# Kernel tuning notes

Measured on AMD Instinct MI355X. Metric: run time of the kernel, lower is better.

Reference implementation:

```python
import jax, jax.numpy as jnp
import numpy as np

N_HEADS = 4
IN_FEATURES = 1024


def setup_inputs() -> dict:
    key = jax.random.key(0)
    ks = jax.random.split(key, 20)
    B, HW, C = 2, 16384, 1024
    inp = {
        "q": jax.random.normal(ks[0], (B, HW, C), dtype=jnp.float32),
        "k": jax.random.normal(ks[1], (B, HW, C), dtype=jnp.float32),
        "v": jax.random.normal(ks[2], (B, HW, C), dtype=jnp.float32),
    }
    names = ["wqg", "bqg", "wkg", "bkg", "wvg", "bvg",
             "wql", "bql", "wkl", "bkl", "wvl", "bvl", "wp", "bp"]
    for i, n in enumerate(names):
        inp[n] = jax.random.normal(ks[3 + i], (C,), dtype=jnp.float32)
    return inp


def _channel_attention(qm, km, vm, scale):
    # qm/km/vm: (b, hw, c). Attention over the CHANNEL dim per head.
    b, n, c = qm.shape
    d = c // N_HEADS
    qh = qm.reshape(b, n, N_HEADS, d).transpose(0, 2, 3, 1)  # (b, H, d, hw)
    kh = km.reshape(b, n, N_HEADS, d).transpose(0, 2, 3, 1)
    vh = vm.reshape(b, n, N_HEADS, d).transpose(0, 2, 3, 1)
    scores = jnp.einsum("bhdn,bhen->bhde", qh, kh) * scale  # (b, H, d, d)
    attn = jax.nn.softmax(scores, axis=-1)
    out = jnp.einsum("bhde,bhen->bhdn", attn, vh)            # (b, H, d, hw)
    return out.transpose(0, 3, 1, 2).reshape(b, n, c)        # (b, hw, c)


def reference(q, k, v, wqg, bqg, wkg, bkg, wvg, bvg,
              wql, bql, wkl, bkl, wvl, bvl, wp, bp):
    scale = IN_FEATURES ** (-0.5)
    # Depthwise (groups==channels, kernel=1) projections: per-channel affine.
    att_global = _channel_attention(q * wqg + bqg, k * wkg + bkg, v * wvg + bvg, scale)
    # window_size=1 -> local patch extraction is identity; local branch uses its own maps.
    att_local = _channel_attention(q * wql + bql, k * wkl + bkl, v * wvl + bvl, scale)
    att = att_global + att_local
    # Both accumulators hold the same att, so projection input is 2*att.
    return (2.0 * att) * wp + bp
```

## Files before the change

kernel.cpp:

```cpp
#include <hip/hip_runtime.h>
#include <stdint.h>

#define NTOK 16384
#define CDIM 1024
#define DHEAD 256

typedef short s16x8 __attribute__((ext_vector_type(8)));
typedef unsigned short u16x8 __attribute__((ext_vector_type(8)));
typedef _Float16 h16x8 __attribute__((ext_vector_type(8)));
typedef float f32x4 __attribute__((ext_vector_type(4)));
typedef float f32x16 __attribute__((ext_vector_type(16)));

static __device__ __forceinline__ unsigned short f2bf(float f) {
    union { float f; unsigned u; } x; x.f = f;
    unsigned r = (x.u + 0x7fffu + ((x.u >> 16) & 1u)) >> 16;
    return (unsigned short)r;
}
static __device__ __forceinline__ unsigned short f2h(float f) {
    _Float16 h = (_Float16)f;
    return __builtin_bit_cast(unsigned short, h);
}
static __device__ __forceinline__ void lgkm_barrier() {
    asm volatile("s_waitcnt lgkmcnt(0)" ::: "memory");
    __builtin_amdgcn_s_barrier();
}

__global__ __launch_bounds__(512, 4)
void k_gram(const float* __restrict__ q, const float* __restrict__ k,
            unsigned short* __restrict__ Gpart, float* __restrict__ Spart, int nchunk)
{
    __shared__ __align__(16) unsigned short ls[(256 + 128) * 32];
    unsigned short* lq = ls;
    unsigned short* lk = ls + 256 * 32;

    const int t      = threadIdx.x;
    const int eh     = blockIdx.x & 1;
    const int pairid = blockIdx.x >> 1;
    const int bh     = pairid / nchunk;
    const int chunk  = pairid - bh * nchunk;
    const int b      = bh >> 2, h = bh & 3;
    const int rows   = NTOK / nchunk;
    const int S      = rows >> 5;
    const int n0c    = chunk * rows;

    const int lane = t & 63, w = t >> 6;
    const int wr = w >> 1;
    const int wc = w & 1;
    const int l31 = lane & 31, g2 = lane >> 5;

    const int qcq = t >> 3, qrg = t & 7;
    const int kcq = t >> 4, krs = t & 15;

    const float* qp = q + ((size_t)b * NTOK + n0c + qrg * 4) * CDIM + h * DHEAD + qcq * 4;
    const float* kp = k + ((size_t)b * NTOK + n0c + krs * 2) * CDIM + h * DHEAD + eh * 128 + kcq * 4;

    f32x4 qv[4], kv[2];
#define QLOAD(sidx) do { const size_t o_ = (size_t)(sidx) * 32 * CDIM;            \
        qv[0] = *reinterpret_cast<const f32x4*>(qp + o_);                          \
        qv[1] = *reinterpret_cast<const f32x4*>(qp + o_ + CDIM);                   \
        qv[2] = *reinterpret_cast<const f32x4*>(qp + o_ + 2 * CDIM);               \
        qv[3] = *reinterpret_cast<const f32x4*>(qp + o_ + 3 * CDIM); } while (0)
#define KLOAD(sidx) do { const size_t o_ = (size_t)(sidx) * 32 * CDIM;            \
        kv[0] = *reinterpret_cast<const f32x4*>(kp + o_);                          \
        kv[1] = *reinterpret_cast<const f32x4*>(kp + o_ + CDIM); } while (0)

    QLOAD(0);
    KLOAD(0);

    float sq[4] = {0.f, 0.f, 0.f, 0.f}, sk[4] = {0.f, 0.f, 0.f, 0.f};
    f32x16 acc[2][2];
#pragma unroll
    for (int r = 0; r < 2; ++r)
#pragma unroll
        for (int c = 0; c < 2; ++c)
#pragma unroll
            for (int j = 0; j < 16; ++j) acc[r][c][j] = 0.f;

    for (int s = 0; s < S; ++s) {
#pragma unroll
        for (int j = 0; j < 4; ++j) {
            const int ch = qcq * 4 + j;
            ushort4 p;
            p.x = f2bf(qv[0][j]); p.y = f2bf(qv[1][j]);
            p.z = f2bf(qv[2][j]); p.w = f2bf(qv[3][j]);
            sq[j] += (qv[0][j] + qv[1][j]) + (qv[2][j] + qv[3][j]);
            *reinterpret_cast<ushort4*>(
                &lq[ch * 32 + (((qrg >> 1) ^ (qcq & 3)) * 8) + (qrg & 1) * 4]) = p;
        }
        if (s + 1 < S) QLOAD(s + 1);

#pragma unroll
        for (int j = 0; j < 4; ++j) {
            const int ch = kcq * 4 + j;
            const unsigned pk = (unsigned)f2bf(kv[0][j]) | ((unsigned)f2bf(kv[1][j]) << 16);
            sk[j] += kv[0][j] + kv[1][j];
            *reinterpret_cast<unsigned*>(
                &lk[ch * 32 + (((krs >> 2) ^ (kcq & 3)) * 8) + (krs & 3) * 2]) = pk;
        }
        if (s + 1 < S) KLOAD(s + 1);

        lgkm_barrier();

#pragma unroll
        for (int kk = 0; kk < 2; ++kk) {
            s16x8 af[2];
#pragma unroll
            for (int r = 0; r < 2; ++r) {
                const int ch   = wr * 64 + r * 32 + l31;
                const int slot = (kk * 2 + g2) ^ ((ch >> 2) & 3);
                af[r] = *reinterpret_cast<const s16x8*>(&lq[ch * 32 + slot * 8]);
            }
#pragma unroll
            for (int c = 0; c < 2; ++c) {
                const int ch   = wc * 64 + c * 32 + l31;
                const int slot = (kk * 2 + g2) ^ ((ch >> 2) & 3);
                const s16x8 bf = *reinterpret_cast<const s16x8*>(&lk[ch * 32 + slot * 8]);
#pragma unroll
                for (int r = 0; r < 2; ++r)
                    acc[r][c] = __builtin_amdgcn_mfma_f32_32x32x16_bf16(af[r], bf, acc[r][c], 0, 0, 0);
            }
        }
        lgkm_barrier();
    }
#undef QLOAD
#undef KLOAD

#pragma unroll
    for (int off = 1; off < 8; off <<= 1)
#pragma unroll
        for (int j = 0; j < 4; ++j) sq[j] += __shfl_xor(sq[j], off);
#pragma unroll
    for (int off = 1; off < 16; off <<= 1)
#pragma unroll
        for (int j = 0; j < 4; ++j) sk[j] += __shfl_xor(sk[j], off);
    float* sp = Spart + (size_t)(bh * nchunk + chunk) * 512;
    if ((t & 7) == 0)
        *reinterpret_cast<float4*>(&sp[qcq * 4]) = make_float4(sq[0], sq[1], sq[2], sq[3]);
    if ((t & 15) == 0)
        *reinterpret_cast<float4*>(&sp[256 + eh * 128 + kcq * 4]) = make_float4(sk[0], sk[1], sk[2], sk[3]);

    unsigned short* gp = Gpart + (size_t)(bh * nchunk + chunk) * 65536;
#pragma unroll
    for (int qtr = 0; qtr < 4; ++qtr) {
        if (wr == qtr) {
#pragma unroll
            for (int r = 0; r < 2; ++r)
#pragma unroll
                for (int c = 0; c < 2; ++c)
#pragma unroll
                    for (int reg = 0; reg < 16; ++reg) {
                        const int de_l = r * 32 + (reg & 3) + 8 * (reg >> 2) + 4 * g2;
                        const int e_l  = wc * 64 + c * 32 + l31;
                        ls[de_l * 128 + e_l] = f2h(acc[r][c][reg]);
                    }
        }
        lgkm_barrier();
        {
            const int de_r = t >> 3, col = (t & 7) * 16;
            unsigned short* dst = gp + (qtr * 64 + de_r) * 256 + eh * 128 + col;
            *reinterpret_cast<u16x8*>(dst)     = *reinterpret_cast<const u16x8*>(&ls[de_r * 128 + col]);
            *reinterpret_cast<u16x8*>(dst + 8) = *reinterpret_cast<const u16x8*>(&ls[de_r * 128 + col + 8]);
        }
        lgkm_barrier();
    }
}

__global__ __launch_bounds__(256)
void k_scores(const unsigned short* __restrict__ Gpart, const float* __restrict__ Spart,
              const float* __restrict__ wqg, const float* __restrict__ bqg,
              const float* __restrict__ wkg, const float* __restrict__ bkg,
              const float* __restrict__ wvg, const float* __restrict__ bvg,
              const float* __restrict__ wql, const float* __restrict__ bql,
              const float* __restrict__ wkl, const float* __restrict__ bkl,
              const float* __restrict__ wvl, const float* __restrict__ bvl,
              const float* __restrict__ wp,  const float* __restrict__ bp,
              unsigned short* __restrict__ Wf, float* __restrict__ beta, int nchunk)
{
    __shared__ float sSq[256], sSk[256];
    const int t  = threadIdx.x;
    const int bh = blockIdx.x >> 5;
    const int rg = blockIdx.x & 31;
    const int h  = bh & 3;

    float aq = 0.f, ak = 0.f;
    for (int c = 0; c < nchunk; ++c) {
        const float* sp = Spart + (size_t)(bh * nchunk + c) * 512;
        aq += sp[t]; ak += sp[256 + t];
    }
    sSq[t] = aq; sSk[t] = ak;
    __syncthreads();

    const int dl  = t >> 5;
    const int de  = rg * 8 + dl;
    const int e8  = (t & 31) * 8;
    const int cd  = h * DHEAD + de;
    const int ce0 = h * DHEAD + e8;

    float g[8] = {0.f, 0.f, 0.f, 0.f, 0.f, 0.f, 0.f, 0.f};
    const unsigned short* gpb = Gpart + (size_t)bh * nchunk * 65536 + (size_t)de * 256 + e8;
    for (int c = 0; c < nchunk; ++c) {
        h16x8 v = *reinterpret_cast<const h16x8*>(gpb + (size_t)c * 65536);
#pragma unroll
        for (int j = 0; j < 8; ++j) g[j] += (float)v[j];
    }

    const float sqv = sSq[de];
    float skv[8];
#pragma unroll
    for (int j = 0; j < 8; ++j) skv[j] = sSk[e8 + j];

    float wrow[8] = {0.f, 0.f, 0.f, 0.f, 0.f, 0.f, 0.f, 0.f};
    float bacc = 0.f;
    const float scale = 0.03125f;
#pragma unroll
    for (int br = 0; br < 2; ++br) {
        const float* wq = br ? wql : wqg;  const float* bq = br ? bql : bqg;
        const float* wk = br ? wkl : wkg;  const float* bk = br ? bkl : bkg;
        const float* wv = br ? wvl : wvg;  const float* bv = br ? bvl : bvg;
        const float wqv = wq[cd], bqv = bq[cd];

        float s[8], m = -1e30f;
#pragma unroll
        for (int j = 0; j < 8; ++j) {
            const float wkv = wk[ce0 + j], bkv = bk[ce0 + j];
            s[j] = scale * (wqv * wkv * g[j] + wqv * bkv * sqv
                            + bqv * wkv * skv[j] + bqv * bkv * 16384.0f);
            m = fmaxf(m, s[j]);
        }
#pragma unroll
        for (int off = 16; off; off >>= 1) m = fmaxf(m, __shfl_xor(m, off));
        float p[8], sum = 0.f;
#pragma unroll
        for (int j = 0; j < 8; ++j) { p[j] = __expf(s[j] - m); sum += p[j]; }
#pragma unroll
        for (int off = 16; off; off >>= 1) sum += __shfl_xor(sum, off);
        const float inv = 1.f / sum;
#pragma unroll
        for (int j = 0; j < 8; ++j) {
            const float a = p[j] * inv;
            wrow[j] += a * wv[ce0 + j];
            bacc    += a * bv[ce0 + j];
        }
    }
    const float wp2 = 2.f * wp[cd];
    u16x8 pw;
#pragma unroll
    for (int j = 0; j < 8; ++j) pw[j] = f2bf(wp2 * wrow[j]);
    const int ks = e8 >> 5, ew = e8 & 31;
    *reinterpret_cast<u16x8*>(Wf + (size_t)bh * 65536 + ((ks * 256 + de) * 32 + ew)) = pw;
#pragma unroll
    for (int off = 16; off; off >>= 1) bacc += __shfl_xor(bacc, off);
    if ((t & 31) == 0) beta[bh * 256 + de] = wp2 * bacc + bp[cd];
}

__global__ __launch_bounds__(512, 4)
void k_out(const float* __restrict__ v, const unsigned short* __restrict__ Wf,
           const float* __restrict__ beta, float* __restrict__ out)
{
    __shared__ __align__(16) unsigned short lv[128 * 256];
    const int t    = threadIdx.x;
    const int bh   = blockIdx.x >> 7;
    const int tile = blockIdx.x & 127;
    const int b    = bh >> 2, h = bh & 3;
    const int n0   = tile * 128;

    const int nr = t >> 5, ch0 = (t & 31) * 8;
    const float* vp = v + ((size_t)b * NTOK + n0 + nr) * CDIM + (size_t)h * DHEAD + ch0;

    f32x4 sA[2], sB[2];
#define VLOAD(dst, i) do { const size_t o_ = (size_t)(i) * 16 * CDIM;              \
        dst[0] = *reinterpret_cast<const f32x4*>(vp + o_);                         \
        dst[1] = *reinterpret_cast<const f32x4*>(vp + o_ + 4); } while (0)

    VLOAD(sA, 0);
    VLOAD(sB, 1);
#pragma unroll
    for (int i = 0; i < 8; i += 2) {
        {
            const int n = i * 16 + nr;
            u16x8 p;
#pragma unroll
            for (int j = 0; j < 4; ++j) { p[j] = f2bf(sA[0][j]); p[4 + j] = f2bf(sA[1][j]); }
            *reinterpret_cast<u16x8*>(&lv[n * 256 + (((t & 31) ^ (n & 7)) * 8)]) = p;
        }
        if (i + 2 < 8) VLOAD(sA, i + 2);
        {
            const int n = (i + 1) * 16 + nr;
            u16x8 p;
#pragma unroll
            for (int j = 0; j < 4; ++j) { p[j] = f2bf(sB[0][j]); p[4 + j] = f2bf(sB[1][j]); }
            *reinterpret_cast<u16x8*>(&lv[n * 256 + (((t & 31) ^ (n & 7)) * 8)]) = p;
        }
        if (i + 3 < 8) VLOAD(sB, i + 3);
    }
#undef VLOAD
    __syncthreads();

    const int w = t >> 6, lane = t & 63, li = lane & 15, g = lane >> 4;
    const int nw  = (w >> 1) * 32;
    const int dd0 = (w & 1) * 128;
    const unsigned short* wf = Wf + (size_t)bh * 65536;

    f32x4 acc[2][8];
#pragma unroll
    for (int r = 0; r < 2; ++r)
#pragma unroll
        for (int c = 0; c < 8; ++c) acc[r][c] = (f32x4){0.f, 0.f, 0.f, 0.f};

#pragma unroll
    for (int ks = 0; ks < 8; ++ks) {
        s16x8 af[2];
#pragma unroll
        for (int r = 0; r < 2; ++r) {
            const int n = nw + r * 16 + li;
            af[r] = *reinterpret_cast<const s16x8*>(&lv[n * 256 + (((ks * 4 + g) ^ (n & 7)) * 8)]);
        }
#pragma unroll
        for (int c = 0; c < 8; ++c) {
            const int dd = dd0 + c * 16 + li;
            const s16x8 bf = *reinterpret_cast<const s16x8*>(wf + ((ks * 256 + dd) * 32 + g * 8));
            acc[0][c] = __builtin_amdgcn_mfma_f32_16x16x32_bf16(af[0], bf, acc[0][c], 0, 0, 0);
            acc[1][c] = __builtin_amdgcn_mfma_f32_16x16x32_bf16(af[1], bf, acc[1][c], 0, 0, 0);
        }
    }

    float betar[8];
#pragma unroll
    for (int c = 0; c < 8; ++c) betar[c] = beta[bh * 256 + dd0 + c * 16 + li];

#pragma unroll
    for (int r = 0; r < 2; ++r)
#pragma unroll
        for (int c = 0; c < 8; ++c) {
            const int dd = dd0 + c * 16 + li;
#pragma unroll
            for (int reg = 0; reg < 4; ++reg) {
                const int n = nw + r * 16 + g * 4 + reg;
                out[((size_t)b * NTOK + n0 + n) * CDIM + (size_t)h * DHEAD + dd] =
                    acc[r][c][reg] + betar[c];
            }
        }
}

extern "C" void kernel_launch(void* const* d_in, const int* in_sizes, int n_in,
                              void* d_out, int out_size, void* d_ws, size_t ws_size,
                              hipStream_t stream)
{
    const float* q = (const float*)d_in[0];
    const float* k = (const float*)d_in[1];
    const float* v = (const float*)d_in[2];
    const float* wgt[14];
    for (int i = 0; i < 14; ++i) wgt[i] = (const float*)d_in[3 + i];
    float* out = (float*)d_out;

    int nchunk = 32;
    while (nchunk > 1) {
        size_t need = (size_t)8 * nchunk * 65536 * 2
                    + (size_t)8 * nchunk * 512 * 4
                    + (size_t)8 * 65536 * 2
                    + (size_t)8 * 256 * 4 + 1024;
        if (need <= ws_size) break;
        nchunk >>= 1;
    }

    char* p = (char*)d_ws;
    unsigned short* Gpart = (unsigned short*)p; p += (size_t)8 * nchunk * 65536 * 2;
    float* Spart = (float*)p;                   p += (size_t)8 * nchunk * 512 * 4;
    unsigned short* Wf = (unsigned short*)p;    p += (size_t)8 * 65536 * 2;
    float* beta  = (float*)p;

    k_gram<<<dim3(8 * nchunk * 2), dim3(512), 0, stream>>>(q, k, Gpart, Spart, nchunk);
    k_scores<<<dim3(8 * 32), dim3(256), 0, stream>>>(
        Gpart, Spart,
        wgt[0], wgt[1], wgt[2], wgt[3], wgt[4], wgt[5],
        wgt[6], wgt[7], wgt[8], wgt[9], wgt[10], wgt[11],
        wgt[12], wgt[13], Wf, beta, nchunk);
    k_out<<<dim3(8 * 128), dim3(512), 0, stream>>>(v, Wf, beta, out);
}
```

Baseline: 180.2 us.

## Restructure gram kernel with warp-specialized loaders and double-buffered register prefetch

The gram kernel now steps through 16-token slices instead of 32 and uses two register prefetch sets, so loads run two steps ahead. Loading is split by thread range: threads 0-255 load q, threads 256-383 load k, and the rest only do MFMA. The LDS layout changes to an XOR-swizzled ushort4 scheme, with fragments built from two 8-byte reads. Occupancy is lowered to 2 blocks per CU and block-to-tile mapping is reordered. The aim is more memory-level parallelism, at the cost of twice as many barriers per token and idle threads during the load phase.

```diff
diff --git a/kernel.cpp b/kernel.cpp
--- a/kernel.cpp
+++ b/kernel.cpp
@@ -25,49 +25,73 @@
     __builtin_amdgcn_s_barrier();
 }
 
-__global__ __launch_bounds__(512, 4)
+__global__ __launch_bounds__(512, 2)
 void k_gram(const float* __restrict__ q, const float* __restrict__ k,
             unsigned short* __restrict__ Gpart, float* __restrict__ Spart, int nchunk)
 {
-    __shared__ __align__(16) unsigned short ls[(256 + 128) * 32];
-    unsigned short* lq = ls;
-    unsigned short* lk = ls + 256 * 32;
-
-    const int t      = threadIdx.x;
-    const int eh     = blockIdx.x & 1;
-    const int pairid = blockIdx.x >> 1;
-    const int bh     = pairid / nchunk;
-    const int chunk  = pairid - bh * nchunk;
-    const int b      = bh >> 2, h = bh & 3;
-    const int rows   = NTOK / nchunk;
-    const int S      = rows >> 5;
-    const int n0c    = chunk * rows;
-
+    __shared__ __align__(16) ushort4 lsbuf[2048];
+    ushort4* lq4 = lsbuf;
+    ushort4* lk4 = lsbuf + 1024;
+
+    const int P   = blockIdx.x;
+    const int t8  = P & 7;
+    const int eh  = (P >> 3) & 1;
+    const int thi = P >> 4;
+    const int T   = thi * 8 + t8;
+    const int bh  = T / nchunk;
+    const int chunk = T - bh * nchunk;
+    const int b = bh >> 2, h = bh & 3;
+    const int rows = NTOK / nchunk;
+    const int S    = rows >> 4;
+    const int n0c  = chunk * rows;
+
+    const int t = threadIdx.x;
     const int lane = t & 63, w = t >> 6;
-    const int wr = w >> 1;
-    const int wc = w & 1;
     const int l31 = lane & 31, g2 = lane >> 5;
-
-    const int qcq = t >> 3, qrg = t & 7;
-    const int kcq = t >> 4, krs = t & 15;
-
-    const float* qp = q + ((size_t)b * NTOK + n0c + qrg * 4) * CDIM + h * DHEAD + qcq * 4;
-    const float* kp = k + ((size_t)b * NTOK + n0c + krs * 2) * CDIM + h * DHEAD + eh * 128 + kcq * 4;
-
-    f32x4 qv[4], kv[2];
-#define QLOAD(sidx) do { const size_t o_ = (size_t)(sidx) * 32 * CDIM;            \
-        qv[0] = *reinterpret_cast<const f32x4*>(qp + o_);                          \
-        qv[1] = *reinterpret_cast<const f32x4*>(qp + o_ + CDIM);                   \
-        qv[2] = *reinterpret_cast<const f32x4*>(qp + o_ + 2 * CDIM);               \
-        qv[3] = *reinterpret_cast<const f32x4*>(qp + o_ + 3 * CDIM); } while (0)
-#define KLOAD(sidx) do { const size_t o_ = (size_t)(sidx) * 32 * CDIM;            \
-        kv[0] = *reinterpret_cast<const f32x4*>(kp + o_);                          \
-        kv[1] = *reinterpret_cast<const f32x4*>(kp + o_ + CDIM); } while (0)
-
-    QLOAD(0);
-    KLOAD(0);
-
-    float sq[4] = {0.f, 0.f, 0.f, 0.f}, sk[4] = {0.f, 0.f, 0.f, 0.f};
+    const int wr = w >> 1, wc = w & 1;
+
+    const bool qt = t < 256;
+    const bool kt = (t >= 256) && (t < 384);
+    const int qcq = t >> 2, qrg = t & 3;
+    const int kid = t - 256;
+    const int kcq = kid >> 2, krg = kid & 3;
+
+    const float* qp = q + ((size_t)(b * NTOK + n0c + qrg * 4)) * CDIM + h * DHEAD + qcq * 4;
+    const float* kp = k + ((size_t)(b * NTOK + n0c + krg * 4)) * CDIM + h * DHEAD + eh * 128 + kcq * 4;
+
+    f32x4 qA[4], qB[4];
+
+#define LOADSET(dst, s) do {                                                  \
+        if (qt) { _Pragma("unroll") for (int j_ = 0; j_ < 4; ++j_)             \
+            dst[j_] = *reinterpret_cast<const f32x4*>(qp + ((size_t)(s) * 16 + j_) * CDIM); } \
+        else if (kt) { _Pragma("unroll") for (int j_ = 0; j_ < 4; ++j_)        \
+            dst[j_] = *reinterpret_cast<const f32x4*>(kp + ((size_t)(s) * 16 + j_) * CDIM); } \
+    } while (0)
+
+    float ssum[4] = {0.f, 0.f, 0.f, 0.f};
+
+#define CONSUME(src) do {                                                     \
+        if (qt) {                                                              \
+            _Pragma("unroll") for (int c_ = 0; c_ < 4; ++c_) {                 \
+                const int ch_ = qcq * 4 + c_;                                  \
+                ushort4 p_;                                                    \
+                p_.x = f2bf(src[0][c_]); p_.y = f2bf(src[1][c_]);              \
+                p_.z = f2bf(src[2][c_]); p_.w = f2bf(src[3][c_]);              \
+                ssum[c_] += (src[0][c_] + src[1][c_]) + (src[2][c_] + src[3][c_]); \
+                lq4[qrg * 256 + (ch_ ^ qrg)] = p_;                             \
+            }                                                                  \
+        } else if (kt) {                                                       \
+            _Pragma("unroll") for (int c_ = 0; c_ < 4; ++c_) {                 \
+                const int ch_ = kcq * 4 + c_;                                  \
+                ushort4 p_;                                                    \
+                p_.x = f2bf(src[0][c_]); p_.y = f2bf(src[1][c_]);              \
+                p_.z = f2bf(src[2][c_]); p_.w = f2bf(src[3][c_]);              \
+                ssum[c_] += (src[0][c_] + src[1][c_]) + (src[2][c_] + src[3][c_]); \
+                lk4[krg * 128 + (ch_ ^ krg)] = p_;                             \
+            }                                                                  \
+        }                                                                      \
+    } while (0)
+
     f32x16 acc[2][2];
 #pragma unroll
     for (int r = 0; r < 2; ++r)
@@ -76,69 +100,64 @@
 #pragma unroll
             for (int j = 0; j < 16; ++j) acc[r][c][j] = 0.f;
 
-    for (int s = 0; s < S; ++s) {
-#pragma unroll
-        for (int j = 0; j < 4; ++j) {
-            const int ch = qcq * 4 + j;
-            ushort4 p;
-            p.x = f2bf(qv[0][j]); p.y = f2bf(qv[1][j]);
-            p.z = f2bf(qv[2][j]); p.w = f2bf(qv[3][j]);
-            sq[j] += (qv[0][j] + qv[1][j]) + (qv[2][j] + qv[3][j]);
-            *reinterpret_cast<ushort4*>(
-                &lq[ch * 32 + (((qrg >> 1) ^ (qcq & 3)) * 8) + (qrg & 1) * 4]) = p;
-        }
-        if (s + 1 < S) QLOAD(s + 1);
-
-#pragma unroll
-        for (int j = 0; j < 4; ++j) {
-            const int ch = kcq * 4 + j;
-            const unsigned pk = (unsigned)f2bf(kv[0][j]) | ((unsigned)f2bf(kv[1][j]) << 16);
-            sk[j] += kv[0][j] + kv[1][j];
-            *reinterpret_cast<unsigned*>(
-                &lk[ch * 32 + (((krs >> 2) ^ (kcq & 3)) * 8) + (krs & 3) * 2]) = pk;
-        }
-        if (s + 1 < S) KLOAD(s + 1);
-
-        lgkm_barrier();
-
-#pragma unroll
-        for (int kk = 0; kk < 2; ++kk) {
-            s16x8 af[2];
-#pragma unroll
-            for (int r = 0; r < 2; ++r) {
-                const int ch   = wr * 64 + r * 32 + l31;
-                const int slot = (kk * 2 + g2) ^ ((ch >> 2) & 3);
-                af[r] = *reinterpret_cast<const s16x8*>(&lq[ch * 32 + slot * 8]);
-            }
-#pragma unroll
-            for (int c = 0; c < 2; ++c) {
-                const int ch   = wc * 64 + c * 32 + l31;
-                const int slot = (kk * 2 + g2) ^ ((ch >> 2) & 3);
-                const s16x8 bf = *reinterpret_cast<const s16x8*>(&lk[ch * 32 + slot * 8]);
-#pragma unroll
-                for (int r = 0; r < 2; ++r)
-                    acc[r][c] = __builtin_amdgcn_mfma_f32_32x32x16_bf16(af[r], bf, acc[r][c], 0, 0, 0);
-            }
-        }
-        lgkm_barrier();
-    }
-#undef QLOAD
-#undef KLOAD
-
-#pragma unroll
-    for (int off = 1; off < 8; off <<= 1)
-#pragma unroll
-        for (int j = 0; j < 4; ++j) sq[j] += __shfl_xor(sq[j], off);
-#pragma unroll
-    for (int off = 1; off < 16; off <<= 1)
-#pragma unroll
-        for (int j = 0; j < 4; ++j) sk[j] += __shfl_xor(sk[j], off);
+    const uint2* lqu = reinterpret_cast<const uint2*>(lq4);
+    const uint2* lku = reinterpret_cast<const uint2*>(lk4);
+    const int gLo = 2 * g2, gHi = 2 * g2 + 1;
+
+#define MFMAPHASE() do {                                                      \
+        s16x8 af_[2], bf_[2];                                                 \
+        _Pragma("unroll") for (int r_ = 0; r_ < 2; ++r_) {                    \
+            const int ch_ = wr * 64 + r_ * 32 + l31;                          \
+            const uint2 lo_ = lqu[gLo * 256 + (ch_ ^ gLo)];                   \
+            const uint2 hi_ = lqu[gHi * 256 + (ch_ ^ gHi)];                   \
+            int4 f_; f_.x = lo_.x; f_.y = lo_.y; f_.z = hi_.x; f_.w = hi_.y;  \
+            af_[r_] = __builtin_bit_cast(s16x8, f_);                          \
+        }                                                                      \
+        _Pragma("unroll") for (int c_ = 0; c_ < 2; ++c_) {                    \
+            const int ch_ = wc * 64 + c_ * 32 + l31;                          \
+            const uint2 lo_ = lku[gLo * 128 + (ch_ ^ gLo)];                   \
+            const uint2 hi_ = lku[gHi * 128 + (ch_ ^ gHi)];                   \
+            int4 f_; f_.x = lo_.x; f_.y = lo_.y; f_.z = hi_.x; f_.w = hi_.y;  \
+            bf_[c_] = __builtin_bit_cast(s16x8, f_);                          \
+        }                                                                      \
+        _Pragma("unroll") for (int r_ = 0; r_ < 2; ++r_)                      \
+            _Pragma("unroll") for (int c_ = 0; c_ < 2; ++c_)                  \
+                acc[r_][c_] = __builtin_amdgcn_mfma_f32_32x32x16_bf16(        \
+                    af_[r_], bf_[c_], acc[r_][c_], 0, 0, 0);                  \
+    } while (0)
+
+    LOADSET(qA, 0);
+    LOADSET(qB, 1);
+
+    for (int s = 0; s < S; s += 2) {
+        CONSUME(qA);
+        if (s + 2 < S) LOADSET(qA, s + 2);
+        lgkm_barrier();
+        MFMAPHASE();
+        lgkm_barrier();
+
+        CONSUME(qB);
+        if (s + 3 < S) LOADSET(qB, s + 3);
+        lgkm_barrier();
+        MFMAPHASE();
+        lgkm_barrier();
+    }
+#undef LOADSET
+#undef CONSUME
+#undef MFMAPHASE
+
+#pragma unroll
+    for (int off = 1; off < 4; off <<= 1)
+#pragma unroll
+        for (int c = 0; c < 4; ++c) ssum[c] += __shfl_xor(ssum[c], off);
     float* sp = Spart + (size_t)(bh * nchunk + chunk) * 512;
-    if ((t & 7) == 0)
-        *reinterpret_cast<float4*>(&sp[qcq * 4]) = make_float4(sq[0], sq[1], sq[2], sq[3]);
-    if ((t & 15) == 0)
-        *reinterpret_cast<float4*>(&sp[256 + eh * 128 + kcq * 4]) = make_float4(sk[0], sk[1], sk[2], sk[3]);
-
+    if (qt && (t & 3) == 0)
+        *reinterpret_cast<float4*>(&sp[qcq * 4]) = make_float4(ssum[0], ssum[1], ssum[2], ssum[3]);
+    if (kt && (kid & 3) == 0)
+        *reinterpret_cast<float4*>(&sp[256 + eh * 128 + kcq * 4]) =
+            make_float4(ssum[0], ssum[1], ssum[2], ssum[3]);
+
+    unsigned short* ls = reinterpret_cast<unsigned short*>(lsbuf);
     unsigned short* gp = Gpart + (size_t)(bh * nchunk + chunk) * 65536;
 #pragma unroll
     for (int qtr = 0; qtr < 4; ++qtr) {
@@ -155,11 +174,12 @@
                     }
         }
         lgkm_barrier();
-        {
-            const int de_r = t >> 3, col = (t & 7) * 16;
-            unsigned short* dst = gp + (qtr * 64 + de_r) * 256 + eh * 128 + col;
-            *reinterpret_cast<u16x8*>(dst)     = *reinterpret_cast<const u16x8*>(&ls[de_r * 128 + col]);
-            *reinterpret_cast<u16x8*>(dst + 8) = *reinterpret_cast<const u16x8*>(&ls[de_r * 128 + col + 8]);
+#pragma unroll
+        for (int i = 0; i < 2; ++i) {
+            const int idx = i * 512 + t;
+            const int row = idx >> 4, col = (idx & 15) * 8;
+            *reinterpret_cast<u16x8*>(gp + (size_t)(qtr * 64 + row) * 256 + eh * 128 + col) =
+                *reinterpret_cast<const u16x8*>(&ls[row * 128 + col]);
         }
         lgkm_barrier();
     }
@@ -219,19 +239,19 @@
         const float* wv = br ? wvl : wvg;  const float* bv = br ? bvl : bvg;
         const float wqv = wq[cd], bqv = bq[cd];
 
-        float s[8], m = -1e30f;
+        float s[8], mm = -1e30f;
 #pragma unroll
         for (int j = 0; j < 8; ++j) {
             const float wkv = wk[ce0 + j], bkv = bk[ce0 + j];
             s[j] = scale * (wqv * wkv * g[j] + wqv * bkv * sqv
                             + bqv * wkv * skv[j] + bqv * bkv * 16384.0f);
-            m = fmaxf(m, s[j]);
-        }
-#pragma unroll
-        for (int off = 16; off; off >>= 1) m = fmaxf(m, __shfl_xor(m, off));
+            mm = fmaxf(mm, s[j]);
+        }
+#pragma unroll
+        for (int off = 16; off; off >>= 1) mm = fmaxf(mm, __shfl_xor(mm, off));
         float p[8], sum = 0.f;
 #pragma unroll
-        for (int j = 0; j < 8; ++j) { p[j] = __expf(s[j] - m); sum += p[j]; }
+        for (int j = 0; j < 8; ++j) { p[j] = __expf(s[j] - mm); sum += p[j]; }
 #pragma unroll
         for (int off = 16; off; off >>= 1) sum += __shfl_xor(sum, off);
         const float inv = 1.f / sum;
```

Result: slower. 225.2 us (+25.0%).
